# Performance work log

Hardware: AMD Instinct MI355X
Metric: run time of the kernel (lower is better)

## Reference

```python
import jax, jax.numpy as jnp
import numpy as np
import math

# Hardware quantization constants (Parameter.* in the original repo)
IP = 8        # Parameter.InputPrecesion
ADCP = 5      # Parameter.ADCPrecision
IE = 1        # Parameter.InputEncoding
ADCMAX = 8.0  # Parameter.ADCMax
K = 3         # kernel_size
STRIDE = 1
PAD = 1


def _quant(x, level, vmax):
    # torch: sep = linspace(0, Max, level); x = sep[searchsorted(sep, x + sep[1]/2) - 1]
    # i.e. round-to-nearest onto a uniform grid, saturating at vmax.
    sep = jnp.linspace(0.0, vmax, level, dtype=x.dtype)
    idx = jnp.searchsorted(sep, x + sep[1] * 0.5) - 1
    return jnp.take(sep, idx, mode='clip')


def _conv(x, w):
    return jax.lax.conv_general_dilated(
        x, w, window_strides=(STRIDE, STRIDE),
        padding=[(PAD, PAD), (PAD, PAD)],
        dimension_numbers=('NCHW', 'OIHW', 'NCHW'))


def setup_inputs() -> dict:
    key = jax.random.key(0)
    kx, kw = jax.random.split(key)
    x = jax.random.uniform(kx, (32, 256, 56, 56), dtype=jnp.float32)  # post-ReLU-like, >= 0
    weight = jax.random.normal(kw, (256, 256, 3, 3), dtype=jnp.float32) * 0.01
    return {"x": x, "weight": weight}


def reference(x, weight):
    # split weight into positive / negative conductance arrays
    pweight = jnp.maximum(weight, 0.0)
    nweight = jnp.maximum(-weight, 0.0)
    # input DAC quantization (input.min() >= 0 branch)
    xq = _quant(x, 2 ** IP, ADCMAX)
    # two convs (quant_dev_back is identity in forward), then ADC requant
    lvl_out = K * K * 2 ** (ADCP + math.ceil(IP / IE))
    outpos = _quant(_conv(xq, pweight), lvl_out, ADCMAX)
    outneg = _quant(_conv(xq, nweight), lvl_out, ADCMAX)
    return outpos - outneg
```

## Files before the change

### kernel.cpp

```cpp
#include <hip/hip_runtime.h>

typedef int int32x4 __attribute__((ext_vector_type(4)));

#define B_ 32
#define C_ 256
#define H_ 56
#define W_ 56
#define HP 58
#define WP 58

static constexpr float QSCALE = 255.0f / 8.0f;
static constexpr float D1 = 8.0f / 255.0f;

static constexpr size_t XQ_BYTES = (size_t)B_ * HP * WP * C_;
static constexpr size_t XQ_SPACE = XQ_BYTES + 32768;
static constexpr size_t WT_SPACE = 38ull * 16384;
static constexpr size_t WS_NEED = XQ_SPACE + WT_SPACE + 2048;

#define XROW 3728
#define XBUF (4 * XROW)

__global__ __launch_bounds__(256) void quant_transpose_i8(const float* __restrict__ x,
                                                          char* __restrict__ Xq) {
  __shared__ unsigned short T[W_ * 256];
  const int h = blockIdx.x;
  const int b = blockIdx.y;
  const int c = threadIdx.x;

  const float4* src = (const float4*)(x + (((size_t)b * C_ + c) * H_ + h) * W_);
#pragma unroll
  for (int i = 0; i < 14; ++i) {
    float4 v = src[i];
    float vals[4] = {v.x, v.y, v.z, v.w};
    const int w0 = i * 4;
#pragma unroll
    for (int j = 0; j < 4; ++j) {
      int n = (int)rintf(vals[j] * QSCALE);
      n = n < 0 ? 0 : (n > 255 ? 255 : n);
      T[(w0 + j) * 256 + c] = (unsigned short)n;
    }
  }
  __syncthreads();

  char* row = Xq + (((size_t)b * HP + (h + 1)) * WP) * 256;
  if (threadIdx.x < 64) {
    *(unsigned int*)(row + threadIdx.x * 4) = 0u;
    *(unsigned int*)(row + (size_t)57 * 256 + threadIdx.x * 4) = 0u;
  }
  const int4 z4 = {0, 0, 0, 0};
  if (h == 0) {
    char* r0 = Xq + (((size_t)b * HP + 0) * WP) * 256;
    for (int i = threadIdx.x; i < WP * 16; i += 256) ((int4*)r0)[i] = z4;
  }
  if (h == 55) {
    char* r57 = Xq + (((size_t)b * HP + 57) * WP) * 256;
    for (int i = threadIdx.x; i < WP * 16; i += 256) ((int4*)r57)[i] = z4;
  }

  const int wid = threadIdx.x >> 6;
  const int lane = threadIdx.x & 63;
#pragma unroll
  for (int p = 0; p < 14; ++p) {
    const int w = p * 4 + wid;
    ushort4 v = *(const ushort4*)&T[w * 256 + lane * 4];
    unsigned int packed = (unsigned int)v.x | ((unsigned int)v.y << 8) |
                          ((unsigned int)v.z << 16) | ((unsigned int)v.w << 24);
    *(unsigned int*)(row + (size_t)(w + 1) * 256 + lane * 4) = packed;
  }
}

__global__ __launch_bounds__(256) void prep_weights_i8(const float* __restrict__ w,
                                                       char* __restrict__ Wt,
                                                       float* __restrict__ oscale) {
  __shared__ __align__(16) float wf[2304];
  __shared__ __align__(16) char Wq[2304];
  __shared__ float red[4];
  __shared__ float sbc;
  const int co = blockIdx.x;
  const int tid = threadIdx.x;

  const float4* src = (const float4*)(w + (size_t)co * 2304);
  float m = 0.f;
  for (int i = tid; i < 576; i += 256) {
    float4 v = src[i];
    *(float4*)&wf[i * 4] = v;
    m = fmaxf(fmaxf(fabsf(v.x), fabsf(v.y)), fmaxf(fmaxf(fabsf(v.z), fabsf(v.w)), m));
  }

#pragma unroll
  for (int off = 32; off; off >>= 1) m = fmaxf(m, __shfl_down(m, off));
  if ((tid & 63) == 0) red[tid >> 6] = m;
  __syncthreads();
  if (tid == 0) {
    m = fmaxf(fmaxf(red[0], red[1]), fmaxf(red[2], red[3]));
    m = fmaxf(m, 1e-20f);
    sbc = m;
    oscale[co] = (m / 127.f) * D1;
  }
  __syncthreads();

  if (tid < 9) {
    const int p = tid;
    const float s = sbc / 127.f;
    const float inv = 1.f / s;
    float carry = 0.f;
    for (int ci = 0; ci < 256; ++ci) {
      float t = wf[ci * 9 + p] + carry;
      float qf = rintf(t * inv);
      qf = fminf(fmaxf(qf, -128.f), 127.f);
      carry = t - qf * s;
      Wq[((ci >> 6) * 9 + p) * 64 + (ci & 63)] = (char)(int)qf;
    }
  }
  __syncthreads();

  if (tid < 144) {
    const int chunk = tid >> 2;
    const int g = tid & 3;
    int4 v = *(const int4*)&Wq[chunk * 64 + (g << 4)];
    *(int4*)(Wt + ((size_t)(chunk * 256 + co)) * 64 + (g << 4)) = v;
  }
}

__global__ __launch_bounds__(256, 2) void conv_mfma_i8(const char* __restrict__ Xq,
                                                       const char* __restrict__ Wt,
                                                       const float* __restrict__ oscale,
                                                       float* __restrict__ out) {
  __shared__ __align__(16) char Xl[2][XBUF];
  const int tid = threadIdx.x;
  const int wid = tid >> 6, lane = tid & 63;
  const int col = lane & 15, hi = lane >> 4;

  const int l = blockIdx.x;
  const int wk = (l & 7) * 112 + (l >> 3);
  const int by = wk % 28;
  const int b = wk / 28;
  const int h0 = 2 * by;

  int banf[7];
#pragma unroll
  for (int nf = 0; nf < 7; ++nf) {
    const int n_out = nf * 16 + col;
    const int r = n_out >= 56 ? 1 : 0;
    banf[nf] = hi * XROW + (r * WP + (n_out - r * 56)) * 16;
  }

  int32x4 acc[4][7];
#pragma unroll
  for (int mf = 0; mf < 4; ++mf)
#pragma unroll
    for (int nf = 0; nf < 7; ++nf) acc[mf][nf] = (int32x4){0, 0, 0, 0};

  const char* xrow = Xq + ((size_t)b * HP + h0) * WP * 256;
  const char* wg = Wt + (size_t)(wid * 4096 + col * 64 + hi * 16);
  char* XlB = (char*)Xl;

  int32x4 Wc0, Wc1, Wc2, Wc3, Wn0, Wn1, Wn2, Wn3;
  int32x4 sr0, sr1, sr2, sr3;

  { const int s = tid;       sr0 = *(const int32x4*)(xrow + (s >> 2) * 256 + (s & 3) * 16); }
  { const int s = 256 + tid; sr1 = *(const int32x4*)(xrow + (s >> 2) * 256 + (s & 3) * 16); }
  { const int s = 512 + tid; sr2 = *(const int32x4*)(xrow + (s >> 2) * 256 + (s & 3) * 16); }
  if (tid < 160) { const int s = 768 + tid;
                   sr3 = *(const int32x4*)(xrow + (s >> 2) * 256 + (s & 3) * 16); }
  Wc0 = *(const int32x4*)(wg);
  Wc1 = *(const int32x4*)(wg + 1024);
  Wc2 = *(const int32x4*)(wg + 2048);
  Wc3 = *(const int32x4*)(wg + 3072);
  Wn0 = *(const int32x4*)(wg + 16384);
  Wn1 = *(const int32x4*)(wg + 16384 + 1024);
  Wn2 = *(const int32x4*)(wg + 16384 + 2048);
  Wn3 = *(const int32x4*)(wg + 16384 + 3072);
  { const int s = tid;       *(int32x4*)(XlB + (s & 3) * XROW + (s >> 2) * 16) = sr0; }
  { const int s = 256 + tid; *(int32x4*)(XlB + (s & 3) * XROW + (s >> 2) * 16) = sr1; }
  { const int s = 512 + tid; *(int32x4*)(XlB + (s & 3) * XROW + (s >> 2) * 16) = sr2; }
  if (tid < 160) { const int s = 768 + tid;
                   *(int32x4*)(XlB + (s & 3) * XROW + (s >> 2) * 16) = sr3; }
  __syncthreads();

#define MSTEP(POS, PROW16)                                                               \
  {                                                                                      \
    __builtin_amdgcn_s_setprio(1);                                                       \
    _Pragma("unroll") for (int nf = 0; nf < 7; ++nf) {                                   \
      int32x4 bb = *(const int32x4*)(XlB + bx[nf] + (PROW16));                           \
      acc[0][nf] = __builtin_amdgcn_mfma_i32_16x16x64_i8(Wc0, bb, acc[0][nf], 0, 0, 0);  \
      acc[1][nf] = __builtin_amdgcn_mfma_i32_16x16x64_i8(Wc1, bb, acc[1][nf], 0, 0, 0);  \
      acc[2][nf] = __builtin_amdgcn_mfma_i32_16x16x64_i8(Wc2, bb, acc[2][nf], 0, 0, 0);  \
      acc[3][nf] = __builtin_amdgcn_mfma_i32_16x16x64_i8(Wc3, bb, acc[3][nf], 0, 0, 0);  \
    }                                                                                    \
    __builtin_amdgcn_s_setprio(0);                                                       \
    Wc0 = Wn0; Wc1 = Wn1; Wc2 = Wn2; Wc3 = Wn3;                                          \
    Wn0 = *(const int32x4*)(wgcc + ((POS) + 2) * 16384);                                 \
    Wn1 = *(const int32x4*)(wgcc + ((POS) + 2) * 16384 + 1024);                          \
    Wn2 = *(const int32x4*)(wgcc + ((POS) + 2) * 16384 + 2048);                          \
    Wn3 = *(const int32x4*)(wgcc + ((POS) + 2) * 16384 + 3072);                          \
  }

  const char* wgcc = wg;
#pragma unroll 1
  for (int cc = 0; cc < 4; ++cc) {
    const bool st = (cc < 3);
    const char* xsrc = xrow + (cc + 1) * 64;
    char* xnxt = XlB + ((cc & 1) ^ 1) * XBUF;
    int bx[7];
#pragma unroll
    for (int nf = 0; nf < 7; ++nf) bx[nf] = banf[nf] + (cc & 1) * XBUF;

    if (st) { const int s = tid;       sr0 = *(const int32x4*)(xsrc + (s >> 2) * 256 + (s & 3) * 16); }
    MSTEP(0, 0)
    if (st) { const int s = 256 + tid; sr1 = *(const int32x4*)(xsrc + (s >> 2) * 256 + (s & 3) * 16); }
    MSTEP(1, 16)
    if (st) { const int s = 512 + tid; sr2 = *(const int32x4*)(xsrc + (s >> 2) * 256 + (s & 3) * 16); }
    MSTEP(2, 32)
    if (st && tid < 160) { const int s = 768 + tid;
                           sr3 = *(const int32x4*)(xsrc + (s >> 2) * 256 + (s & 3) * 16); }
    MSTEP(3, 928)
    if (st) { const int s = tid;       *(int32x4*)(xnxt + (s & 3) * XROW + (s >> 2) * 16) = sr0; }
    MSTEP(4, 944)
    if (st) { const int s = 256 + tid; *(int32x4*)(xnxt + (s & 3) * XROW + (s >> 2) * 16) = sr1; }
    MSTEP(5, 960)
    if (st) { const int s = 512 + tid; *(int32x4*)(xnxt + (s & 3) * XROW + (s >> 2) * 16) = sr2; }
    MSTEP(6, 1856)
    if (st && tid < 160) { const int s = 768 + tid;
                           *(int32x4*)(xnxt + (s & 3) * XROW + (s >> 2) * 16) = sr3; }
    MSTEP(7, 1872)
    MSTEP(8, 1888)
    if (st) __syncthreads();
    wgcc += 9 * 16384;
  }
#undef MSTEP

#pragma unroll
  for (int mf = 0; mf < 4; ++mf) {
    const int cbase = wid * 64 + mf * 16 + hi * 4;
    const float4 os = *(const float4*)(oscale + cbase);
#pragma unroll
    for (int nf = 0; nf < 7; ++nf) {
      const int n_out = nf * 16 + col;
      const int r = n_out >= 56 ? 1 : 0;
      const int hrow = h0 + r;
      const int wcol = n_out - r * 56;
      float* o = out + ((((size_t)b * 256 + cbase) * 56 + hrow) * 56 + wcol);
      o[0 * 3136] = (float)acc[mf][nf][0] * os.x;
      o[1 * 3136] = (float)acc[mf][nf][1] * os.y;
      o[2 * 3136] = (float)acc[mf][nf][2] * os.z;
      o[3 * 3136] = (float)acc[mf][nf][3] * os.w;
    }
  }
}

__global__ void conv_naive(const float* __restrict__ x, const float* __restrict__ w,
                           float* __restrict__ out, int total) {
  int idx = blockIdx.x * 256 + threadIdx.x;
  if (idx >= total) return;
  const int wc = idx % 56;
  int t = idx / 56;
  const int hr = t % 56; t /= 56;
  const int co = t % 256;
  const int b = t / 256;
  float acc = 0.f;
  for (int ci = 0; ci < 256; ++ci) {
    const float* xb = x + (((size_t)b * 256 + ci) * 56) * 56;
    const float* wb = w + ((size_t)co * 256 + ci) * 9;
#pragma unroll
    for (int kh = 0; kh < 3; ++kh) {
      const int hh = hr + kh - 1;
      if (hh < 0 || hh >= 56) continue;
#pragma unroll
      for (int kw = 0; kw < 3; ++kw) {
        const int ww = wc + kw - 1;
        if (ww < 0 || ww >= 56) continue;
        const float q = rintf(xb[hh * 56 + ww] * QSCALE) * D1;
        acc += q * wb[kh * 3 + kw];
      }
    }
  }
  out[idx] = acc;
}

extern "C" void kernel_launch(void* const* d_in, const int* in_sizes, int n_in,
                              void* d_out, int out_size, void* d_ws, size_t ws_size,
                              hipStream_t stream) {
  (void)in_sizes; (void)n_in; (void)out_size;
  const float* x = (const float*)d_in[0];
  const float* w = (const float*)d_in[1];
  float* out = (float*)d_out;

  if (ws_size < WS_NEED) {
    const int total = B_ * C_ * H_ * W_;
    conv_naive<<<(total + 255) / 256, 256, 0, stream>>>(x, w, out, total);
    return;
  }

  char* Xq = (char*)d_ws;
  char* Wt = (char*)d_ws + XQ_SPACE;
  float* oscale = (float*)((char*)d_ws + XQ_SPACE + WT_SPACE);

  quant_transpose_i8<<<dim3(56, 32), 256, 0, stream>>>(x, Xq);
  prep_weights_i8<<<dim3(256), 256, 0, stream>>>(w, Wt, oscale);
  conv_mfma_i8<<<dim3(896), 256, 0, stream>>>(Xq, Wt, oscale, out);
}
```

Before: 102.2 us.

## Use planar channel-group layout, direct global-to-LDS loads, and split output channels

The quantised input is stored as 16-channel planes per batch, with the padding border written by the transpose kernel. The conv kernel now fills its shared-memory tiles with global_load_lds instead of staging through registers. Each block covers only half the output channels, which doubles the grid to 1792 blocks, halves the accumulators, and raises launch bounds to 4 blocks per CU for more occupancy and latency hiding. In exchange, every input tile is loaded twice from global or L2 memory (once per channel half), so input traffic doubles.

Result: faster. 94.00 us (-8.0%).

```diff
diff --git a/kernel.cpp b/kernel.cpp
--- a/kernel.cpp
+++ b/kernel.cpp
@@ -6,26 +6,36 @@
 #define C_ 256
 #define H_ 56
 #define W_ 56
-#define HP 58
-#define WP 58
 
 static constexpr float QSCALE = 255.0f / 8.0f;
 static constexpr float D1 = 8.0f / 255.0f;
 
-static constexpr size_t XQ_BYTES = (size_t)B_ * HP * WP * C_;
+#define PLANE 53824
+#define BSTR  861184
+static constexpr size_t XQ_BYTES = (size_t)B_ * BSTR;
 static constexpr size_t XQ_SPACE = XQ_BYTES + 32768;
 static constexpr size_t WT_SPACE = 38ull * 16384;
 static constexpr size_t WS_NEED = XQ_SPACE + WT_SPACE + 2048;
 
-#define XROW 3728
-#define XBUF (4 * XROW)
+#define XROWB 3712
+#define XBUFB 14848
+
+__device__ __forceinline__ void gload_lds16(const void* g, void* l) {
+  __builtin_amdgcn_global_load_lds((const __attribute__((address_space(1))) unsigned int*)g,
+                                   (__attribute__((address_space(3))) unsigned int*)l,
+                                   16, 0, 0);
+}
 
 __global__ __launch_bounds__(256) void quant_transpose_i8(const float* __restrict__ x,
                                                           char* __restrict__ Xq) {
-  __shared__ unsigned short T[W_ * 256];
+  __shared__ __align__(16) char T8[58 * 272];
   const int h = blockIdx.x;
   const int b = blockIdx.y;
-  const int c = threadIdx.x;
+  const int tid = threadIdx.x;
+  const int c = tid;
+
+  T8[0 * 272 + c] = 0;
+  T8[57 * 272 + c] = 0;
 
   const float4* src = (const float4*)(x + (((size_t)b * C_ + c) * H_ + h) * W_);
 #pragma unroll
@@ -37,35 +47,30 @@
     for (int j = 0; j < 4; ++j) {
       int n = (int)rintf(vals[j] * QSCALE);
       n = n < 0 ? 0 : (n > 255 ? 255 : n);
-      T[(w0 + j) * 256 + c] = (unsigned short)n;
-    }
-  }
-  __syncthreads();
-
-  char* row = Xq + (((size_t)b * HP + (h + 1)) * WP) * 256;
-  if (threadIdx.x < 64) {
-    *(unsigned int*)(row + threadIdx.x * 4) = 0u;
-    *(unsigned int*)(row + (size_t)57 * 256 + threadIdx.x * 4) = 0u;
-  }
-  const int4 z4 = {0, 0, 0, 0};
-  if (h == 0) {
-    char* r0 = Xq + (((size_t)b * HP + 0) * WP) * 256;
-    for (int i = threadIdx.x; i < WP * 16; i += 256) ((int4*)r0)[i] = z4;
-  }
-  if (h == 55) {
-    char* r57 = Xq + (((size_t)b * HP + 57) * WP) * 256;
-    for (int i = threadIdx.x; i < WP * 16; i += 256) ((int4*)r57)[i] = z4;
-  }
-
-  const int wid = threadIdx.x >> 6;
-  const int lane = threadIdx.x & 63;
-#pragma unroll
-  for (int p = 0; p < 14; ++p) {
-    const int w = p * 4 + wid;
-    ushort4 v = *(const ushort4*)&T[w * 256 + lane * 4];
-    unsigned int packed = (unsigned int)v.x | ((unsigned int)v.y << 8) |
-                          ((unsigned int)v.z << 16) | ((unsigned int)v.w << 24);
-    *(unsigned int*)(row + (size_t)(w + 1) * 256 + lane * 4) = packed;
+      T8[(w0 + j + 1) * 272 + c] = (char)n;
+    }
+  }
+  __syncthreads();
+
+  char* Xb = Xq + (size_t)b * BSTR;
+#pragma unroll
+  for (int p = 0; p < 4; ++p) {
+    if (tid < 232) {
+      const int w = tid % 58;
+      const int cig = p * 4 + tid / 58;
+      *(int4*)(Xb + (size_t)cig * PLANE + (h + 1) * 928 + w * 16) =
+          *(const int4*)&T8[w * 272 + cig * 16];
+    }
+  }
+
+  if (h == 0 || h == 55) {
+    const int hb = (h == 0) ? 0 : 57;
+    const int4 z = {0, 0, 0, 0};
+    for (int i = tid; i < 928; i += 256) {
+      const int w = i % 58;
+      const int cig = i / 58;
+      *(int4*)(Xb + (size_t)cig * PLANE + hb * 928 + w * 16) = z;
+    }
   }
 }
 
@@ -122,19 +127,21 @@
   }
 }
 
-__global__ __launch_bounds__(256, 2) void conv_mfma_i8(const char* __restrict__ Xq,
+__global__ __launch_bounds__(256, 4) void conv_mfma_i8(const char* __restrict__ Xq,
                                                        const char* __restrict__ Wt,
                                                        const float* __restrict__ oscale,
                                                        float* __restrict__ out) {
-  __shared__ __align__(16) char Xl[2][XBUF];
+  __shared__ __align__(16) char Xl[2][XBUFB];
   const int tid = threadIdx.x;
   const int wid = tid >> 6, lane = tid & 63;
   const int col = lane & 15, hi = lane >> 4;
 
   const int l = blockIdx.x;
-  const int wk = (l & 7) * 112 + (l >> 3);
-  const int by = wk % 28;
-  const int b = wk / 28;
+  const int wk = (l & 7) * 224 + (l >> 3);
+  const int mh = wk & 1;
+  const int rest = wk >> 1;
+  const int by = rest % 28;
+  const int b = rest / 28;
   const int h0 = 2 * by;
 
   int banf[7];
@@ -142,87 +149,65 @@
   for (int nf = 0; nf < 7; ++nf) {
     const int n_out = nf * 16 + col;
     const int r = n_out >= 56 ? 1 : 0;
-    banf[nf] = hi * XROW + (r * WP + (n_out - r * 56)) * 16;
-  }
-
-  int32x4 acc[4][7];
-#pragma unroll
-  for (int mf = 0; mf < 4; ++mf)
+    banf[nf] = hi * XROWB + (r * 58 + (n_out - r * 56)) * 16;
+  }
+
+  int32x4 acc[2][7];
+#pragma unroll
+  for (int mf = 0; mf < 2; ++mf)
 #pragma unroll
     for (int nf = 0; nf < 7; ++nf) acc[mf][nf] = (int32x4){0, 0, 0, 0};
 
-  const char* xrow = Xq + ((size_t)b * HP + h0) * WP * 256;
-  const char* wg = Wt + (size_t)(wid * 4096 + col * 64 + hi * 16);
-  char* XlB = (char*)Xl;
-
-  int32x4 Wc0, Wc1, Wc2, Wc3, Wn0, Wn1, Wn2, Wn3;
-  int32x4 sr0, sr1, sr2, sr3;
-
-  { const int s = tid;       sr0 = *(const int32x4*)(xrow + (s >> 2) * 256 + (s & 3) * 16); }
-  { const int s = 256 + tid; sr1 = *(const int32x4*)(xrow + (s >> 2) * 256 + (s & 3) * 16); }
-  { const int s = 512 + tid; sr2 = *(const int32x4*)(xrow + (s >> 2) * 256 + (s & 3) * 16); }
-  if (tid < 160) { const int s = 768 + tid;
-                   sr3 = *(const int32x4*)(xrow + (s >> 2) * 256 + (s & 3) * 16); }
+  const char* Xqb = Xq + (size_t)b * BSTR + h0 * 928;
+  const char* wg = Wt + (size_t)((mh * 128 + wid * 32 + col) * 64 + hi * 16);
+
+  int32x4 Wc0, Wc1, Wn0, Wn1;
+
+#pragma unroll
+  for (int q = 0; q < 4; ++q)
+    if (tid < 232) gload_lds16(Xqb + (size_t)q * PLANE + tid * 16,
+                               (char*)Xl + q * XROWB + tid * 16);
   Wc0 = *(const int32x4*)(wg);
   Wc1 = *(const int32x4*)(wg + 1024);
-  Wc2 = *(const int32x4*)(wg + 2048);
-  Wc3 = *(const int32x4*)(wg + 3072);
   Wn0 = *(const int32x4*)(wg + 16384);
   Wn1 = *(const int32x4*)(wg + 16384 + 1024);
-  Wn2 = *(const int32x4*)(wg + 16384 + 2048);
-  Wn3 = *(const int32x4*)(wg + 16384 + 3072);
-  { const int s = tid;       *(int32x4*)(XlB + (s & 3) * XROW + (s >> 2) * 16) = sr0; }
-  { const int s = 256 + tid; *(int32x4*)(XlB + (s & 3) * XROW + (s >> 2) * 16) = sr1; }
-  { const int s = 512 + tid; *(int32x4*)(XlB + (s & 3) * XROW + (s >> 2) * 16) = sr2; }
-  if (tid < 160) { const int s = 768 + tid;
-                   *(int32x4*)(XlB + (s & 3) * XROW + (s >> 2) * 16) = sr3; }
   __syncthreads();
 
 #define MSTEP(POS, PROW16)                                                               \
   {                                                                                      \
     __builtin_amdgcn_s_setprio(1);                                                       \
     _Pragma("unroll") for (int nf = 0; nf < 7; ++nf) {                                   \
-      int32x4 bb = *(const int32x4*)(XlB + bx[nf] + (PROW16));                           \
+      int32x4 bb = *(const int32x4*)(xl + banf[nf] + (PROW16));                          \
       acc[0][nf] = __builtin_amdgcn_mfma_i32_16x16x64_i8(Wc0, bb, acc[0][nf], 0, 0, 0);  \
       acc[1][nf] = __builtin_amdgcn_mfma_i32_16x16x64_i8(Wc1, bb, acc[1][nf], 0, 0, 0);  \
-      acc[2][nf] = __builtin_amdgcn_mfma_i32_16x16x64_i8(Wc2, bb, acc[2][nf], 0, 0, 0);  \
-      acc[3][nf] = __builtin_amdgcn_mfma_i32_16x16x64_i8(Wc3, bb, acc[3][nf], 0, 0, 0);  \
     }                                                                                    \
     __builtin_amdgcn_s_setprio(0);                                                       \
-    Wc0 = Wn0; Wc1 = Wn1; Wc2 = Wn2; Wc3 = Wn3;                                          \
+    Wc0 = Wn0; Wc1 = Wn1;                                                                \
     Wn0 = *(const int32x4*)(wgcc + ((POS) + 2) * 16384);                                 \
     Wn1 = *(const int32x4*)(wgcc + ((POS) + 2) * 16384 + 1024);                          \
-    Wn2 = *(const int32x4*)(wgcc + ((POS) + 2) * 16384 + 2048);                          \
-    Wn3 = *(const int32x4*)(wgcc + ((POS) + 2) * 16384 + 3072);                          \
   }
 
   const char* wgcc = wg;
 #pragma unroll 1
   for (int cc = 0; cc < 4; ++cc) {
     const bool st = (cc < 3);
-    const char* xsrc = xrow + (cc + 1) * 64;
-    char* xnxt = XlB + ((cc & 1) ^ 1) * XBUF;
-    int bx[7];
-#pragma unroll
-    for (int nf = 0; nf < 7; ++nf) bx[nf] = banf[nf] + (cc & 1) * XBUF;
-
-    if (st) { const int s = tid;       sr0 = *(const int32x4*)(xsrc + (s >> 2) * 256 + (s & 3) * 16); }
+    const char* xl = (const char*)Xl + (cc & 1) * XBUFB;
+    char* xnxt = (char*)Xl + ((cc & 1) ^ 1) * XBUFB;
+    const char* xsrc = Xqb + (size_t)(4 * (cc + 1)) * PLANE;
+
+    if (st && tid < 232) gload_lds16(xsrc + tid * 16, xnxt + tid * 16);
     MSTEP(0, 0)
-    if (st) { const int s = 256 + tid; sr1 = *(const int32x4*)(xsrc + (s >> 2) * 256 + (s & 3) * 16); }
+    if (st && tid < 232) gload_lds16(xsrc + (size_t)PLANE + tid * 16, xnxt + XROWB + tid * 16);
     MSTEP(1, 16)
-    if (st) { const int s = 512 + tid; sr2 = *(const int32x4*)(xsrc + (s >> 2) * 256 + (s & 3) * 16); }
+    if (st && tid < 232) gload_lds16(xsrc + 2 * (size_t)PLANE + tid * 16,
+                                     xnxt + 2 * XROWB + tid * 16);
     MSTEP(2, 32)
-    if (st && tid < 160) { const int s = 768 + tid;
-                           sr3 = *(const int32x4*)(xsrc + (s >> 2) * 256 + (s & 3) * 16); }
+    if (st && tid < 232) gload_lds16(xsrc + 3 * (size_t)PLANE + tid * 16,
+                                     xnxt + 3 * XROWB + tid * 16);
     MSTEP(3, 928)
-    if (st) { const int s = tid;       *(int32x4*)(xnxt + (s & 3) * XROW + (s >> 2) * 16) = sr0; }
     MSTEP(4, 944)
-    if (st) { const int s = 256 + tid; *(int32x4*)(xnxt + (s & 3) * XROW + (s >> 2) * 16) = sr1; }
     MSTEP(5, 960)
-    if (st) { const int s = 512 + tid; *(int32x4*)(xnxt + (s & 3) * XROW + (s >> 2) * 16) = sr2; }
     MSTEP(6, 1856)
-    if (st && tid < 160) { const int s = 768 + tid;
-                           *(int32x4*)(xnxt + (s & 3) * XROW + (s >> 2) * 16) = sr3; }
     MSTEP(7, 1872)
     MSTEP(8, 1888)
     if (st) __syncthreads();
@@ -231,8 +216,8 @@
 #undef MSTEP
 
 #pragma unroll
-  for (int mf = 0; mf < 4; ++mf) {
-    const int cbase = wid * 64 + mf * 16 + hi * 4;
+  for (int mf = 0; mf < 2; ++mf) {
+    const int cbase = mh * 128 + wid * 32 + mf * 16 + hi * 4;
     const float4 os = *(const float4*)(oscale + cbase);
 #pragma unroll
     for (int nf = 0; nf < 7; ++nf) {
@@ -298,5 +283,5 @@
 
   quant_transpose_i8<<<dim3(56, 32), 256, 0, stream>>>(x, Xq);
   prep_weights_i8<<<dim3(256), 256, 0, stream>>>(w, Wt, oscale);
-  conv_mfma_i8<<<dim3(896), 256, 0, stream>>>(Xq, Wt, oscale, out);
-}
+  conv_mfma_i8<<<dim3(1792), 256, 0, stream>>>(Xq, Wt, oscale, out);
+}
```
